# Kernel tuning notes

Hardware: AMD Instinct MI355X
Metric: run time of the kernel (lower is better)

## Reference

```python
import jax, jax.numpy as jnp
import numpy as np

NUM_HEADS = 32
HEAD_DIM = 128
HEAVY_BUDGET = 256
RECENT_BUDGET = 256
ROPE_BASE = 10000.0


def _rope_tables(position_ids, head_dim, dtype):
    inv_freq = 1.0 / (ROPE_BASE ** (jnp.arange(0, head_dim, 2, dtype=jnp.float32) / head_dim))
    freqs = position_ids.astype(jnp.float32)[..., None] * inv_freq  # [b, s, hd/2]
    emb = jnp.concatenate([freqs, freqs], axis=-1)                  # [b, s, hd]
    return jnp.cos(emb).astype(dtype), jnp.sin(emb).astype(dtype)


def _rotate_half(x):
    h = x.shape[-1] // 2
    return jnp.concatenate([-x[..., h:], x[..., :h]], axis=-1)


def setup_inputs() -> dict:
    key = jax.random.key(0)
    k1, k2, k3, k4, k5 = jax.random.split(key, 5)
    b, s, d = 1, 2048, 4096
    hidden_states = jax.random.normal(k1, (b, s, d), dtype=jnp.float32)
    # additive causal mask, as HF passes into forward
    neg = jnp.finfo(jnp.float32).min
    causal = jnp.tril(jnp.ones((s, s), dtype=bool))
    attention_mask = jnp.where(causal, 0.0, neg).astype(jnp.float32)[None, None]  # [1,1,s,s]
    position_ids = jnp.arange(s, dtype=jnp.int32)[None]  # [1, s]
    scale = 0.02
    Wq = jax.random.normal(k2, (d, d), dtype=jnp.float32) * scale
    Wk = jax.random.normal(k3, (d, d), dtype=jnp.float32) * scale
    Wv = jax.random.normal(k4, (d, d), dtype=jnp.float32) * scale
    Wo = jax.random.normal(k5, (d, d), dtype=jnp.float32) * scale
    return {"hidden_states": hidden_states, "attention_mask": attention_mask,
            "position_ids": position_ids, "Wq": Wq, "Wk": Wk, "Wv": Wv, "Wo": Wo}


def reference(hidden_states, attention_mask, position_ids, Wq, Wk, Wv, Wo):
    b, s, d = hidden_states.shape
    H, hd = NUM_HEADS, HEAD_DIM
    kv = s  # prefill: no past_key_value, masks reset

    # projections: nn.Linear(x) = x @ W.T
    q = (hidden_states @ Wq.T).reshape(b, s, H, hd).transpose(0, 2, 1, 3)  # [b,H,s,hd]
    k = (hidden_states @ Wk.T).reshape(b, s, H, hd).transpose(0, 2, 1, 3)
    v = (hidden_states @ Wv.T).reshape(b, s, H, hd).transpose(0, 2, 1, 3)

    cos, sin = _rope_tables(position_ids, hd, q.dtype)  # [b,s,hd]
    cos, sin = cos[:, None], sin[:, None]               # broadcast over heads
    q = q * cos + _rotate_half(q) * sin
    k = k * cos + _rotate_half(k) * sin

    attn = jnp.einsum('bhqd,bhkd->bhqk', q, k) / np.float32(np.sqrt(hd))
    neg = jnp.finfo(attn.dtype).min
    attn = jnp.maximum(attn + attention_mask, neg)
    # attention_masks_next is None on the first (prefill) call -> no multiplicative mask here
    attn = jax.nn.softmax(attn.astype(jnp.float32), axis=-1).astype(q.dtype)  # [b,H,s,kv]

    # running per-head score accumulation: sum over batch and query dims
    scores = attn.sum(axis=0).sum(axis=1)  # [H, kv]; previous_scores is None at prefill

    # heavy-hitter eviction mask for the next decode step (kv+1 columns)
    mask = jnp.ones((H, kv + 1), dtype=attn.dtype)
    # attn_tokens_all (=kv) > cache_budget, recent_budget > 0:
    mask = mask.at[:, :kv + 1 - RECENT_BUDGET].set(0.0)
    selected = scores[:, :kv - RECENT_BUDGET]                    # drop recent region
    _, keep_topk = jax.lax.top_k(selected, HEAVY_BUDGET)         # [H, heavy]
    mask = mask.at[jnp.arange(H)[:, None], keep_topk].set(1.0)   # scatter heavy hitters
    # torch aliasing: score_mask = attn_mask[:, :-1]; score_mask[:, -recent:] = 1 mutates attn_mask too
    mask = mask.at[:, kv - RECENT_BUDGET:kv].set(1.0)
    attention_masks_next = mask[None, :, None, :]                # [1,H,1,kv+1]
    previous_scores = scores * mask[:, :kv]                      # masked score state

    out = jnp.einsum('bhqk,bhkd->bhqd', attn, v)                 # [b,H,s,hd]
    out = out.transpose(0, 2, 1, 3).reshape(b, s, d) @ Wo.T
    return out, attention_masks_next, previous_scores
```

## Files before the change

kernel.cpp:

```cpp
#include <hip/hip_runtime.h>
#include <hip/hip_bf16.h>
#include <cmath>

#define S_LEN 2048
#define DMODEL 4096
#define NH 32
#define HDIM 128
#define HEAVY 256
#define RECENT 256
#define ATTN_SCALE 0.08838834764831845f
#define NEGBIG -3.0e38f
#define MB (1024ull * 1024ull)

typedef __attribute__((ext_vector_type(8))) short short8v;
typedef __attribute__((ext_vector_type(4))) short short4v;
typedef __attribute__((ext_vector_type(4))) float floatx4;

__device__ inline ushort f2bf(float x) {
  __hip_bfloat16 h = __float2bfloat16(x);
  return __builtin_bit_cast(ushort, h);
}
struct Split3 {
  short a, b, c;
};
__device__ inline Split3 split3(float x) {
  unsigned u = __float_as_uint(x);
  unsigned u1 = u & 0xFFFF0000u;
  float r1 = x - __uint_as_float(u1);
  unsigned u2 = __float_as_uint(r1) & 0xFFFF0000u;
  float r2 = r1 - __uint_as_float(u2);
  unsigned u3 = __float_as_uint(r2);
  Split3 o;
  o.a = (short)(u1 >> 16);
  o.b = (short)(u2 >> 16);
  o.c = (short)(u3 >> 16);
  return o;
}

__device__ __forceinline__ void gl_lds16(const short* gsrc, short* ldst) {
  __builtin_amdgcn_global_load_lds((const __attribute__((address_space(1))) void*)gsrc,
                                   (__attribute__((address_space(3))) void*)ldst, 16, 0, 0);
}

__global__ void split_mat(const float* __restrict__ X, short* __restrict__ Xa,
                          short* __restrict__ Xb, short* __restrict__ Xc, int n4) {
  int stride = gridDim.x * blockDim.x;
  for (int i = blockIdx.x * blockDim.x + threadIdx.x; i < n4; i += stride) {
    float4 v = reinterpret_cast<const float4*>(X)[i];
    float vv[4] = {v.x, v.y, v.z, v.w};
    short4v a, b, c;
#pragma unroll
    for (int j = 0; j < 4; j++) {
      Split3 t = split3(vv[j]);
      a[j] = t.a; b[j] = t.b; c[j] = t.c;
    }
    reinterpret_cast<short4v*>(Xa)[i] = a;
    reinterpret_cast<short4v*>(Xb)[i] = b;
    reinterpret_cast<short4v*>(Xc)[i] = c;
  }
}

__global__ __launch_bounds__(256) void gemm6h(const short* __restrict__ Aag,
                                              const short* __restrict__ Abg,
                                              const short* __restrict__ Acg,
                                              const float* __restrict__ B,
                                              float* __restrict__ C, int M, int N, int K) {
  __shared__ short Aa[128 * 40], Ab[128 * 40], Ac[128 * 40];
  __shared__ short Ba[128 * 40], Bb[128 * 40], Bc[128 * 40];
  const int tid = threadIdx.x;
  const int w = tid >> 6, l = tid & 63, g = l >> 4, ln = l & 15;
  const int wm = w >> 1, wn = w & 1;
  const int row0 = blockIdx.y * 128, col0 = blockIdx.x * 128;
  floatx4 acc[4][4] = {};
  for (int k0 = 0; k0 < K; k0 += 32) {
    __syncthreads();
#pragma unroll
    for (int i = 0; i < 2; i++) {
      int id = tid + i * 256;
      int r = id >> 2, c = id & 3;
      size_t ga = (size_t)(row0 + r) * K + k0 + c * 8;
      int o = r * 40 + c * 8;
      *reinterpret_cast<short8v*>(&Aa[o]) = *reinterpret_cast<const short8v*>(&Aag[ga]);
      *reinterpret_cast<short8v*>(&Ab[o]) = *reinterpret_cast<const short8v*>(&Abg[ga]);
      *reinterpret_cast<short8v*>(&Ac[o]) = *reinterpret_cast<const short8v*>(&Acg[ga]);
    }
#pragma unroll
    for (int i = 0; i < 4; i++) {
      int id = tid + i * 256;
      int r = id >> 3, c4 = id & 7;
      float4 bv = *reinterpret_cast<const float4*>(&B[(size_t)(col0 + r) * K + k0 + c4 * 4]);
      float bf[4] = {bv.x, bv.y, bv.z, bv.w};
      short4v b1, b2, b3;
#pragma unroll
      for (int j = 0; j < 4; j++) {
        Split3 t = split3(bf[j]);
        b1[j] = t.a; b2[j] = t.b; b3[j] = t.c;
      }
      int o = r * 40 + c4 * 4;
      *reinterpret_cast<short4v*>(&Ba[o]) = b1;
      *reinterpret_cast<short4v*>(&Bb[o]) = b2;
      *reinterpret_cast<short4v*>(&Bc[o]) = b3;
    }
    __syncthreads();
#pragma unroll
    for (int i = 0; i < 4; i++) {
      int ar = (wm * 64 + i * 16 + ln) * 40 + g * 8;
      short8v a1 = *reinterpret_cast<const short8v*>(&Aa[ar]);
      short8v a2 = *reinterpret_cast<const short8v*>(&Ab[ar]);
      short8v a3 = *reinterpret_cast<const short8v*>(&Ac[ar]);
#pragma unroll
      for (int j = 0; j < 4; j++) {
        int br = (wn * 64 + j * 16 + ln) * 40 + g * 8;
        short8v b1 = *reinterpret_cast<const short8v*>(&Ba[br]);
        short8v b2 = *reinterpret_cast<const short8v*>(&Bb[br]);
        short8v b3 = *reinterpret_cast<const short8v*>(&Bc[br]);
        acc[i][j] = __builtin_amdgcn_mfma_f32_16x16x32_bf16(a1, b1, acc[i][j], 0, 0, 0);
        acc[i][j] = __builtin_amdgcn_mfma_f32_16x16x32_bf16(a1, b2, acc[i][j], 0, 0, 0);
        acc[i][j] = __builtin_amdgcn_mfma_f32_16x16x32_bf16(a2, b1, acc[i][j], 0, 0, 0);
        acc[i][j] = __builtin_amdgcn_mfma_f32_16x16x32_bf16(a1, b3, acc[i][j], 0, 0, 0);
        acc[i][j] = __builtin_amdgcn_mfma_f32_16x16x32_bf16(a2, b2, acc[i][j], 0, 0, 0);
        acc[i][j] = __builtin_amdgcn_mfma_f32_16x16x32_bf16(a3, b1, acc[i][j], 0, 0, 0);
      }
    }
  }
#pragma unroll
  for (int i = 0; i < 4; i++)
#pragma unroll
    for (int j = 0; j < 4; j++)
#pragma unroll
      for (int r = 0; r < 4; r++)
        C[(size_t)(row0 + wm * 64 + i * 16 + g * 4 + r) * N + col0 + wn * 64 + j * 16 + ln] =
            acc[i][j][r];
}

__global__ __launch_bounds__(256) void gemm_bf1(const float* __restrict__ A,
                                                const float* __restrict__ B,
                                                float* __restrict__ C, int M, int N, int K) {
  __shared__ short Ah[128 * 40];
  __shared__ short Bh[128 * 40];
  const int tid = threadIdx.x;
  const int w = tid >> 6, l = tid & 63, g = l >> 4, ln = l & 15;
  const int wm = w >> 1, wn = w & 1;
  const int row0 = blockIdx.y * 128, col0 = blockIdx.x * 128;
  floatx4 acc[4][4] = {};
  for (int k0 = 0; k0 < K; k0 += 32) {
    __syncthreads();
#pragma unroll
    for (int i = 0; i < 4; i++) {
      int id = tid + i * 256;
      int r = id >> 3, c4 = id & 7;
      float4 av = *reinterpret_cast<const float4*>(&A[(size_t)(row0 + r) * K + k0 + c4 * 4]);
      float4 bv = *reinterpret_cast<const float4*>(&B[(size_t)(col0 + r) * K + k0 + c4 * 4]);
      short4v ah, bh;
      ah[0] = (short)f2bf(av.x); ah[1] = (short)f2bf(av.y);
      ah[2] = (short)f2bf(av.z); ah[3] = (short)f2bf(av.w);
      bh[0] = (short)f2bf(bv.x); bh[1] = (short)f2bf(bv.y);
      bh[2] = (short)f2bf(bv.z); bh[3] = (short)f2bf(bv.w);
      *reinterpret_cast<short4v*>(&Ah[r * 40 + c4 * 4]) = ah;
      *reinterpret_cast<short4v*>(&Bh[r * 40 + c4 * 4]) = bh;
    }
    __syncthreads();
#pragma unroll
    for (int i = 0; i < 4; i++) {
      short8v a = *reinterpret_cast<const short8v*>(&Ah[(wm * 64 + i * 16 + ln) * 40 + g * 8]);
#pragma unroll
      for (int j = 0; j < 4; j++) {
        short8v b = *reinterpret_cast<const short8v*>(&Bh[(wn * 64 + j * 16 + ln) * 40 + g * 8]);
        acc[i][j] = __builtin_amdgcn_mfma_f32_16x16x32_bf16(a, b, acc[i][j], 0, 0, 0);
      }
    }
  }
#pragma unroll
  for (int i = 0; i < 4; i++)
#pragma unroll
    for (int j = 0; j < 4; j++)
#pragma unroll
      for (int r = 0; r < 4; r++)
        C[(size_t)(row0 + wm * 64 + i * 16 + g * 4 + r) * N + col0 + wn * 64 + j * 16 + ln] =
            acc[i][j][r];
}

__global__ __launch_bounds__(256) void gemm_vbt(const short* __restrict__ Ab2,
                                                const float* __restrict__ B,
                                                ushort* __restrict__ Vt, int M, int N, int K) {
  __shared__ short Ah[128 * 40];
  __shared__ short Bh[128 * 40];
  const int tid = threadIdx.x;
  const int w = tid >> 6, l = tid & 63, g = l >> 4, ln = l & 15;
  const int wm = w >> 1, wn = w & 1;
  const int row0 = blockIdx.y * 128, col0 = blockIdx.x * 128;
  floatx4 acc[4][4] = {};
  for (int k0 = 0; k0 < K; k0 += 32) {
    __syncthreads();
#pragma unroll
    for (int i = 0; i < 2; i++) {
      int id = tid + i * 256;
      int r = id >> 2, c = id & 3;
      *reinterpret_cast<short8v*>(&Ah[r * 40 + c * 8]) =
          *reinterpret_cast<const short8v*>(&Ab2[(size_t)(row0 + r) * K + k0 + c * 8]);
    }
#pragma unroll
    for (int i = 0; i < 4; i++) {
      int id = tid + i * 256;
      int r = id >> 3, c4 = id & 7;
      float4 bv = *reinterpret_cast<const float4*>(&B[(size_t)(col0 + r) * K + k0 + c4 * 4]);
      short4v bh;
      bh[0] = (short)f2bf(bv.x); bh[1] = (short)f2bf(bv.y);
      bh[2] = (short)f2bf(bv.z); bh[3] = (short)f2bf(bv.w);
      *reinterpret_cast<short4v*>(&Bh[r * 40 + c4 * 4]) = bh;
    }
    __syncthreads();
#pragma unroll
    for (int i = 0; i < 4; i++) {
      short8v a = *reinterpret_cast<const short8v*>(&Ah[(wm * 64 + i * 16 + ln) * 40 + g * 8]);
#pragma unroll
      for (int j = 0; j < 4; j++) {
        short8v b = *reinterpret_cast<const short8v*>(&Bh[(wn * 64 + j * 16 + ln) * 40 + g * 8]);
        acc[i][j] = __builtin_amdgcn_mfma_f32_16x16x32_bf16(a, b, acc[i][j], 0, 0, 0);
      }
    }
  }
#pragma unroll
  for (int i = 0; i < 4; i++)
#pragma unroll
    for (int j = 0; j < 4; j++) {
      short4v o;
#pragma unroll
      for (int r = 0; r < 4; r++) o[r] = (short)f2bf(acc[i][j][r]);
      size_t n = col0 + wn * 64 + j * 16 + ln;
      size_t m0 = row0 + wm * 64 + i * 16 + g * 4;
      *reinterpret_cast<short4v*>(&Vt[n * M + m0]) = o;
    }
}

__global__ void rope_convert(const float* __restrict__ Q, const float* __restrict__ K,
                             const int* __restrict__ pos, short* __restrict__ Qa,
                             short* __restrict__ Qb, short* __restrict__ Qc,
                             short* __restrict__ Ka, short* __restrict__ Kb,
                             short* __restrict__ Kc) {
  int idx = blockIdx.x * blockDim.x + threadIdx.x;
  if (idx >= S_LEN * 64) return;
  int d = idx & 63;
  int r = idx >> 6;
  float p = (float)pos[r];
  float invf = (float)pow(10000.0, -(double)(2 * d) / 128.0);
  float ang = p * invf;
  float c = cosf(ang), s = sinf(ang);
  for (int h = 0; h < NH; h++) {
    size_t base = (size_t)r * DMODEL + h * HDIM + d;
    float q1 = Q[base], q2 = Q[base + 64];
    float k1 = K[base], k2 = K[base + 64];
    float qa = q1 * c - q2 * s, qb = q2 * c + q1 * s;
    float ka = k1 * c - k2 * s, kb = k2 * c + k1 * s;
    Split3 t;
    t = split3(qa); Qa[base] = t.a; Qb[base] = t.b; Qc[base] = t.c;
    t = split3(qb); Qa[base + 64] = t.a; Qb[base + 64] = t.b; Qc[base + 64] = t.c;
    t = split3(ka); Ka[base] = t.a; Kb[base] = t.b; Kc[base] = t.c;
    t = split3(kb); Ka[base + 64] = t.a; Kb[base + 64] = t.b; Kc[base + 64] = t.c;
  }
}

#define KVB 32
#define KSPL (KVB * 128)

__device__ __forceinline__ floatx4 qk6_tile(const short* KaS, const short* KbS,
                                            const short* KcS, const short8v q1[4],
                                            const short8v q2[4], const short8v q3[4],
                                            int krow, int g) {
  floatx4 cA = {}, cB = {}, cC = {}, cD = {}, cE = {}, cF = {};
#pragma unroll
  for (int dc = 0; dc < 4; dc++) {
    int didx = krow * 128 + ((dc * 32 + g * 8) ^ ((krow & 7) << 3));
    short8v k1 = *reinterpret_cast<const short8v*>(&KaS[didx]);
    short8v k2 = *reinterpret_cast<const short8v*>(&KbS[didx]);
    short8v k3 = *reinterpret_cast<const short8v*>(&KcS[didx]);
    cA = __builtin_amdgcn_mfma_f32_16x16x32_bf16(q1[dc], k1, cA, 0, 0, 0);
    cB = __builtin_amdgcn_mfma_f32_16x16x32_bf16(q1[dc], k2, cB, 0, 0, 0);
    cC = __builtin_amdgcn_mfma_f32_16x16x32_bf16(q2[dc], k1, cC, 0, 0, 0);
    cD = __builtin_amdgcn_mfma_f32_16x16x32_bf16(q1[dc], k3, cD, 0, 0, 0);
    cE = __builtin_amdgcn_mfma_f32_16x16x32_bf16(q2[dc], k2, cE, 0, 0, 0);
    cF = __builtin_amdgcn_mfma_f32_16x16x32_bf16(q3[dc], k1, cF, 0, 0, 0);
  }
  return ((cA + cB) + (cC + cD)) + (cE + cF);
}

__device__ __forceinline__ void issue_tile(const short* __restrict__ Ka,
                                           const short* __restrict__ Kb,
                                           const short* __restrict__ Kc, int k0, int h,
                                           short* bufA, short* bufB, short* bufC, int tid) {
  const int wb = tid & 192;
#pragma unroll
  for (int it = 0; it < 2; it++) {
    int j = it * 256 + tid;
    int r = j >> 4, cl = j & 15;
    int cg = cl ^ (r & 7);
    size_t goff = (size_t)(k0 + r) * DMODEL + h * HDIM + cg * 8;
    int cb = (it * 256 + wb) * 8;
    gl_lds16(Ka + goff, bufA + cb);
    gl_lds16(Kb + goff, bufB + cb);
    gl_lds16(Kc + goff, bufC + cb);
  }
}

__global__ __launch_bounds__(256, 3) void attn_fused(
    const short* __restrict__ Qa, const short* __restrict__ Qb, const short* __restrict__ Qc,
    const short* __restrict__ Ka, const short* __restrict__ Kb, const short* __restrict__ Kc,
    const ushort* __restrict__ Vt, float* __restrict__ AO, float* __restrict__ sp4) {
  __shared__ short KS[2][3][KSPL];
  __shared__ short Ps[4 * 512];
  const int bid = blockIdx.x;
  const int qb = 31 - (bid >> 5);
  const int h = bid & 31;
  const int tid = threadIdx.x;
  const int w = tid >> 6, g = (tid >> 4) & 3, ln = tid & 15;
  const int q0 = qb * 64;
  const int qrow = q0 + w * 16 + ln;
  short8v q1[4], q2[4], q3[4];
#pragma unroll
  for (int dc = 0; dc < 4; dc++) {
    size_t off = (size_t)qrow * DMODEL + h * HDIM + dc * 32 + g * 8;
    q1[dc] = *reinterpret_cast<const short8v*>(&Qa[off]);
    q2[dc] = *reinterpret_cast<const short8v*>(&Qb[off]);
    q3[dc] = *reinterpret_cast<const short8v*>(&Qc[off]);
  }
  float m_r[4], l_r[4];
#pragma unroll
  for (int r = 0; r < 4; r++) { m_r[r] = NEGBIG; l_r[r] = 0.f; }
  const int nkt = 2 * qb + 2;

  issue_tile(Ka, Kb, Kc, 0, h, KS[0][0], KS[0][1], KS[0][2], tid);
  __syncthreads();
  for (int t = 0; t < nkt; t++) {
    const int k0 = t * KVB;
    const int cur = t & 1;
    if (t + 1 < nkt)
      issue_tile(Ka, Kb, Kc, k0 + KVB, h, KS[cur ^ 1][0], KS[cur ^ 1][1], KS[cur ^ 1][2], tid);
    float sv[2][4];
#pragma unroll
    for (int ct = 0; ct < 2; ct++) {
      floatx4 sacc = qk6_tile(KS[cur][0], KS[cur][1], KS[cur][2], q1, q2, q3, ct * 16 + ln, g);
#pragma unroll
      for (int r = 0; r < 4; r++) {
        float s = sacc[r] * ATTN_SCALE;
        int key = k0 + ct * 16 + ln;
        int qq = q0 + w * 16 + g * 4 + r;
        sv[ct][r] = (key <= qq) ? s : NEGBIG;
      }
    }
#pragma unroll
    for (int r = 0; r < 4; r++) {
      float tmax = fmaxf(sv[0][r], sv[1][r]);
      tmax = fmaxf(tmax, __shfl_xor(tmax, 1));
      tmax = fmaxf(tmax, __shfl_xor(tmax, 2));
      tmax = fmaxf(tmax, __shfl_xor(tmax, 4));
      tmax = fmaxf(tmax, __shfl_xor(tmax, 8));
      float mnew = fmaxf(m_r[r], tmax);
      float ssum = __expf(sv[0][r] - mnew) + __expf(sv[1][r] - mnew);
      ssum += __shfl_xor(ssum, 1);
      ssum += __shfl_xor(ssum, 2);
      ssum += __shfl_xor(ssum, 4);
      ssum += __shfl_xor(ssum, 8);
      l_r[r] = l_r[r] * __expf(m_r[r] - mnew) + ssum;
      m_r[r] = mnew;
    }
    __syncthreads();
  }
  float inv_l[4];
#pragma unroll
  for (int r = 0; r < 4; r++) inv_l[r] = 1.0f / l_r[r];

  floatx4 o[8] = {};
  issue_tile(Ka, Kb, Kc, 0, h, KS[0][0], KS[0][1], KS[0][2], tid);
  __syncthreads();
  for (int t = 0; t < nkt; t++) {
    const int k0 = t * KVB;
    const int cur = t & 1;
    if (t + 1 < nkt)
      issue_tile(Ka, Kb, Kc, k0 + KVB, h, KS[cur ^ 1][0], KS[cur ^ 1][1], KS[cur ^ 1][2], tid);
    float pv[2][4];
#pragma unroll
    for (int ct = 0; ct < 2; ct++) {
      floatx4 sacc = qk6_tile(KS[cur][0], KS[cur][1], KS[cur][2], q1, q2, q3, ct * 16 + ln, g);
#pragma unroll
      for (int r = 0; r < 4; r++) {
        float s = sacc[r] * ATTN_SCALE;
        int key = k0 + ct * 16 + ln;
        int qq = q0 + w * 16 + g * 4 + r;
        s = (key <= qq) ? s : NEGBIG;
        pv[ct][r] = __expf(s - m_r[r]) * inv_l[r];
      }
    }
#pragma unroll
    for (int ct = 0; ct < 2; ct++) {
      float c2 = pv[ct][0] + pv[ct][1] + pv[ct][2] + pv[ct][3];
      c2 += __shfl_xor(c2, 16);
      c2 += __shfl_xor(c2, 32);
      if (g == 0) sp4[((size_t)(qb * 4 + w) * NH + h) * S_LEN + k0 + ct * 16 + ln] = c2;
    }
#pragma unroll
    for (int ct = 0; ct < 2; ct++)
#pragma unroll
      for (int r = 0; r < 4; r++) {
        int prow = g * 4 + r, pcol = ct * 16 + ln;
        Ps[w * 512 + prow * 32 + (pcol ^ (((prow >> 1) & 1) << 4))] = (short)f2bf(pv[ct][r]);
      }
    short8v pa = *reinterpret_cast<const short8v*>(
        &Ps[w * 512 + ln * 32 + ((g * 8) ^ (((ln >> 1) & 1) << 4))]);
#pragma unroll
    for (int ctd = 0; ctd < 8; ctd++) {
      size_t voff = ((size_t)h * HDIM + ctd * 16 + ln) * S_LEN + k0 + g * 8;
      short8v vb = *reinterpret_cast<const short8v*>(&Vt[voff]);
      o[ctd] = __builtin_amdgcn_mfma_f32_16x16x32_bf16(pa, vb, o[ctd], 0, 0, 0);
    }
    __syncthreads();
  }
#pragma unroll
  for (int ctd = 0; ctd < 8; ctd++)
#pragma unroll
    for (int r = 0; r < 4; r++)
      AO[(size_t)(q0 + w * 16 + g * 4 + r) * DMODEL + h * HDIM + ctd * 16 + ln] = o[ctd][r];
}

__global__ void reduce_scores(const float* __restrict__ sp4, float* __restrict__ scores) {
  int idx = blockIdx.x * blockDim.x + threadIdx.x;
  if (idx >= NH * S_LEN) return;
  int h = idx >> 11, k = idx & 2047;
  float s = 0.f;
  for (int j = 0; j < 128; j++) s += sp4[((size_t)j * NH + h) * S_LEN + k];
  scores[idx] = s;
}

__global__ __launch_bounds__(256) void topk_mask_kernel(const float* __restrict__ scores,
                                                        float* __restrict__ out_mask,
                                                        float* __restrict__ prev_scores) {
  const int h = blockIdx.x;
  __shared__ unsigned sb[S_LEN - RECENT];
  __shared__ int cnt_sh;
  const int NSEL = S_LEN - RECENT;
  const int tid = threadIdx.x;
  const float* sc = scores + (size_t)h * S_LEN;
  for (int i = tid; i < NSEL; i += 256) sb[i] = __float_as_uint(sc[i]);
  __syncthreads();
  unsigned prefix = 0u;
  for (int b = 31; b >= 0; b--) {
    unsigned cand = prefix | (1u << b);
    if (tid == 0) cnt_sh = 0;
    __syncthreads();
    int c = 0;
    for (int i = tid; i < NSEL; i += 256) c += (sb[i] >= cand) ? 1 : 0;
    atomicAdd(&cnt_sh, c);
    __syncthreads();
    if (cnt_sh >= HEAVY) prefix = cand;
    __syncthreads();
  }
  if (tid == 0) cnt_sh = 0;
  __syncthreads();
  int c = 0;
  for (int i = tid; i < NSEL; i += 256) c += (sb[i] > prefix) ? 1 : 0;
  atomicAdd(&cnt_sh, c);
  __syncthreads();
  const int c1 = cnt_sh;
  float* mrow = out_mask + (size_t)h * (S_LEN + 1);
  float* prow = prev_scores + (size_t)h * S_LEN;
  for (int j = NSEL + tid; j < S_LEN + 1; j += 256) mrow[j] = 1.0f;
  for (int k = NSEL + tid; k < S_LEN; k += 256) prow[k] = sc[k];
  for (int i = tid; i < NSEL; i += 256) {
    bool sel = sb[i] > prefix;
    mrow[i] = sel ? 1.f : 0.f;
    prow[i] = sel ? sc[i] : 0.f;
  }
  __syncthreads();
  if (tid == 0) {
    int need = HEAVY - c1;
    for (int i = 0; i < NSEL && need > 0; i++) {
      if (sb[i] == prefix) { mrow[i] = 1.f; prow[i] = sc[i]; need--; }
    }
  }
}

extern "C" void kernel_launch(void* const* d_in, const int* in_sizes, int n_in,
                              void* d_out, int out_size, void* d_ws, size_t ws_size,
                              hipStream_t stream) {
  const float* hidden = (const float*)d_in[0];
  const int* pos = (const int*)d_in[2];
  const float* Wq = (const float*)d_in[3];
  const float* Wk = (const float*)d_in[4];
  const float* Wv = (const float*)d_in[5];
  const float* Wo = (const float*)d_in[6];

  float* out0 = (float*)d_out;
  float* out_mask = out0 + (size_t)S_LEN * DMODEL;
  float* prev_scores = out_mask + (size_t)NH * (S_LEN + 1);

  char* ws = (char*)d_ws;
  float* Qf = (float*)(ws + 0 * MB);
  float* Kf = (float*)(ws + 32 * MB);
  ushort* Vt = (ushort*)(ws + 64 * MB);
  short* Ha = (short*)(ws + 80 * MB);
  short* Hb = (short*)(ws + 96 * MB);
  short* Hc = (short*)(ws + 112 * MB);
  short* Qa = (short*)(ws + 80 * MB);
  short* Qb = (short*)(ws + 96 * MB);
  short* Qc = (short*)(ws + 112 * MB);
  short* Ka = (short*)(ws + 128 * MB);
  short* Kb = (short*)(ws + 144 * MB);
  short* Kc = (short*)(ws + 160 * MB);
  float* AO = Qf;
  float* sp4 = Kf;
  float* scores = (float*)(ws + 64 * MB);

  dim3 gg(DMODEL / 128, S_LEN / 128);
  split_mat<<<2048, 256, 0, stream>>>(hidden, Ha, Hb, Hc, S_LEN * DMODEL / 4);
  gemm6h<<<gg, 256, 0, stream>>>(Ha, Hb, Hc, Wq, Qf, S_LEN, DMODEL, DMODEL);
  gemm6h<<<gg, 256, 0, stream>>>(Ha, Hb, Hc, Wk, Kf, S_LEN, DMODEL, DMODEL);
  gemm_vbt<<<gg, 256, 0, stream>>>(Ha, Wv, Vt, S_LEN, DMODEL, DMODEL);

  int rope_total = S_LEN * 64;
  rope_convert<<<(rope_total + 255) / 256, 256, 0, stream>>>(Qf, Kf, pos, Qa, Qb, Qc, Ka, Kb, Kc);

  hipError_t _e = hipMemsetAsync(sp4, 0, (size_t)128 * NH * S_LEN * sizeof(float), stream);
  (void)_e;
  attn_fused<<<1024, 256, 0, stream>>>(Qa, Qb, Qc, Ka, Kb, Kc, Vt, AO, sp4);

  reduce_scores<<<(NH * S_LEN + 255) / 256, 256, 0, stream>>>(sp4, scores);
  topk_mask_kernel<<<NH, 256, 0, stream>>>(scores, out_mask, prev_scores);

  gemm_bf1<<<gg, 256, 0, stream>>>(AO, Wo, out0, S_LEN, DMODEL, DMODEL);
}
```

Measured before the change: 1.594 ms.

## Pre-split Q/K weights into bf16 triples and use a Cauchy-Schwarz softmax bound

Q and K weights are now split into three bf16 parts in separate passes, half a matrix at a time, so the GEMM loads ready-made bf16 B tiles instead of re-splitting fp32 weights in every block. A new norms kernel computes per-row query norms and a per-head max key norm. Attention then uses |q|·max|k|·scale as a fixed upper bound in place of the online running max, which removes the per-tile max and sum shuffle reductions from the first pass. The cost is extra split passes and workspace traffic. The fixed bound also risks exp underflow when real scores sit far below it.

```diff
diff --git a/kernel.cpp b/kernel.cpp
--- a/kernel.cpp
+++ b/kernel.cpp
@@ -60,17 +60,36 @@
   }
 }
 
-__global__ __launch_bounds__(256) void gemm6h(const short* __restrict__ Aag,
-                                              const short* __restrict__ Abg,
-                                              const short* __restrict__ Acg,
-                                              const float* __restrict__ B,
-                                              float* __restrict__ C, int M, int N, int K) {
+__global__ void norms_kernel(const float* __restrict__ Qf, const float* __restrict__ Kf,
+                             float* __restrict__ qn, unsigned* __restrict__ mk2) {
+  int p = blockIdx.x * 4 + (threadIdx.x >> 6);
+  int lane = threadIdx.x & 63;
+  int r = p >> 5, h = p & 31;
+  const float2 qv = *reinterpret_cast<const float2*>(&Qf[(size_t)r * DMODEL + h * HDIM + lane * 2]);
+  const float2 kv = *reinterpret_cast<const float2*>(&Kf[(size_t)r * DMODEL + h * HDIM + lane * 2]);
+  float sq = qv.x * qv.x + qv.y * qv.y;
+  float sk = kv.x * kv.x + kv.y * kv.y;
+#pragma unroll
+  for (int off = 1; off <= 32; off <<= 1) {
+    sq += __shfl_xor(sq, off);
+    sk += __shfl_xor(sk, off);
+  }
+  if (lane == 0) {
+    qn[h * S_LEN + r] = sqrtf(sq);
+    atomicMax(&mk2[h], __float_as_uint(sk));
+  }
+}
+
+__global__ __launch_bounds__(256) void gemm6p(
+    const short* __restrict__ Aag, const short* __restrict__ Abg, const short* __restrict__ Acg,
+    const short* __restrict__ Bag, const short* __restrict__ Bbg, const short* __restrict__ Bcg,
+    float* __restrict__ C, int M, int N, int K, int colbase) {
   __shared__ short Aa[128 * 40], Ab[128 * 40], Ac[128 * 40];
   __shared__ short Ba[128 * 40], Bb[128 * 40], Bc[128 * 40];
   const int tid = threadIdx.x;
   const int w = tid >> 6, l = tid & 63, g = l >> 4, ln = l & 15;
   const int wm = w >> 1, wn = w & 1;
-  const int row0 = blockIdx.y * 128, col0 = blockIdx.x * 128;
+  const int row0 = blockIdx.y * 128, col0l = blockIdx.x * 128;
   floatx4 acc[4][4] = {};
   for (int k0 = 0; k0 < K; k0 += 32) {
     __syncthreads();
@@ -79,27 +98,14 @@
       int id = tid + i * 256;
       int r = id >> 2, c = id & 3;
       size_t ga = (size_t)(row0 + r) * K + k0 + c * 8;
+      size_t gb = (size_t)(col0l + r) * K + k0 + c * 8;
       int o = r * 40 + c * 8;
       *reinterpret_cast<short8v*>(&Aa[o]) = *reinterpret_cast<const short8v*>(&Aag[ga]);
       *reinterpret_cast<short8v*>(&Ab[o]) = *reinterpret_cast<const short8v*>(&Abg[ga]);
       *reinterpret_cast<short8v*>(&Ac[o]) = *reinterpret_cast<const short8v*>(&Acg[ga]);
-    }
-#pragma unroll
-    for (int i = 0; i < 4; i++) {
-      int id = tid + i * 256;
-      int r = id >> 3, c4 = id & 7;
-      float4 bv = *reinterpret_cast<const float4*>(&B[(size_t)(col0 + r) * K + k0 + c4 * 4]);
-      float bf[4] = {bv.x, bv.y, bv.z, bv.w};
-      short4v b1, b2, b3;
-#pragma unroll
-      for (int j = 0; j < 4; j++) {
-        Split3 t = split3(bf[j]);
-        b1[j] = t.a; b2[j] = t.b; b3[j] = t.c;
-      }
-      int o = r * 40 + c4 * 4;
-      *reinterpret_cast<short4v*>(&Ba[o]) = b1;
-      *reinterpret_cast<short4v*>(&Bb[o]) = b2;
-      *reinterpret_cast<short4v*>(&Bc[o]) = b3;
+      *reinterpret_cast<short8v*>(&Ba[o]) = *reinterpret_cast<const short8v*>(&Bag[gb]);
+      *reinterpret_cast<short8v*>(&Bb[o]) = *reinterpret_cast<const short8v*>(&Bbg[gb]);
+      *reinterpret_cast<short8v*>(&Bc[o]) = *reinterpret_cast<const short8v*>(&Bcg[gb]);
     }
     __syncthreads();
 #pragma unroll
@@ -123,6 +129,7 @@
       }
     }
   }
+  const int col0 = colbase + col0l;
 #pragma unroll
   for (int i = 0; i < 4; i++)
 #pragma unroll
@@ -305,7 +312,8 @@
 __global__ __launch_bounds__(256, 3) void attn_fused(
     const short* __restrict__ Qa, const short* __restrict__ Qb, const short* __restrict__ Qc,
     const short* __restrict__ Ka, const short* __restrict__ Kb, const short* __restrict__ Kc,
-    const ushort* __restrict__ Vt, float* __restrict__ AO, float* __restrict__ sp4) {
+    const ushort* __restrict__ Vt, const float* __restrict__ qn,
+    const unsigned* __restrict__ mk2, float* __restrict__ AO, float* __restrict__ sp4) {
   __shared__ short KS[2][3][KSPL];
   __shared__ short Ps[4 * 512];
   const int bid = blockIdx.x;
@@ -323,9 +331,13 @@
     q2[dc] = *reinterpret_cast<const short8v*>(&Qb[off]);
     q3[dc] = *reinterpret_cast<const short8v*>(&Qc[off]);
   }
-  float m_r[4], l_r[4];
-#pragma unroll
-  for (int r = 0; r < 4; r++) { m_r[r] = NEGBIG; l_r[r] = 0.f; }
+  const float mk = sqrtf(__uint_as_float(mk2[h]));
+  float B_r[4], l_r[4];
+#pragma unroll
+  for (int r = 0; r < 4; r++) {
+    B_r[r] = qn[h * S_LEN + q0 + w * 16 + g * 4 + r] * mk * ATTN_SCALE;
+    l_r[r] = 0.f;
+  }
   const int nkt = 2 * qb + 2;
 
   issue_tile(Ka, Kb, Kc, 0, h, KS[0][0], KS[0][1], KS[0][2], tid);
@@ -335,7 +347,6 @@
     const int cur = t & 1;
     if (t + 1 < nkt)
       issue_tile(Ka, Kb, Kc, k0 + KVB, h, KS[cur ^ 1][0], KS[cur ^ 1][1], KS[cur ^ 1][2], tid);
-    float sv[2][4];
 #pragma unroll
     for (int ct = 0; ct < 2; ct++) {
       floatx4 sacc = qk6_tile(KS[cur][0], KS[cur][1], KS[cur][2], q1, q2, q3, ct * 16 + ln, g);
@@ -344,30 +355,21 @@
         float s = sacc[r] * ATTN_SCALE;
         int key = k0 + ct * 16 + ln;
         int qq = q0 + w * 16 + g * 4 + r;
-        sv[ct][r] = (key <= qq) ? s : NEGBIG;
+        l_r[r] += (key <= qq) ? __expf(s - B_r[r]) : 0.f;
       }
     }
-#pragma unroll
-    for (int r = 0; r < 4; r++) {
-      float tmax = fmaxf(sv[0][r], sv[1][r]);
-      tmax = fmaxf(tmax, __shfl_xor(tmax, 1));
-      tmax = fmaxf(tmax, __shfl_xor(tmax, 2));
-      tmax = fmaxf(tmax, __shfl_xor(tmax, 4));
-      tmax = fmaxf(tmax, __shfl_xor(tmax, 8));
-      float mnew = fmaxf(m_r[r], tmax);
-      float ssum = __expf(sv[0][r] - mnew) + __expf(sv[1][r] - mnew);
-      ssum += __shfl_xor(ssum, 1);
-      ssum += __shfl_xor(ssum, 2);
-      ssum += __shfl_xor(ssum, 4);
-      ssum += __shfl_xor(ssum, 8);
-      l_r[r] = l_r[r] * __expf(m_r[r] - mnew) + ssum;
-      m_r[r] = mnew;
-    }
     __syncthreads();
   }
   float inv_l[4];
 #pragma unroll
-  for (int r = 0; r < 4; r++) inv_l[r] = 1.0f / l_r[r];
+  for (int r = 0; r < 4; r++) {
+    float l = l_r[r];
+    l += __shfl_xor(l, 1);
+    l += __shfl_xor(l, 2);
+    l += __shfl_xor(l, 4);
+    l += __shfl_xor(l, 8);
+    inv_l[r] = 1.0f / l;
+  }
 
   floatx4 o[8] = {};
   issue_tile(Ka, Kb, Kc, 0, h, KS[0][0], KS[0][1], KS[0][2], tid);
@@ -386,8 +388,8 @@
         float s = sacc[r] * ATTN_SCALE;
         int key = k0 + ct * 16 + ln;
         int qq = q0 + w * 16 + g * 4 + r;
-        s = (key <= qq) ? s : NEGBIG;
-        pv[ct][r] = __expf(s - m_r[r]) * inv_l[r];
+        float e = (key <= qq) ? __expf(s - B_r[r]) : 0.f;
+        pv[ct][r] = e * inv_l[r];
       }
     }
 #pragma unroll
@@ -502,6 +504,9 @@
   short* Qa = (short*)(ws + 80 * MB);
   short* Qb = (short*)(ws + 96 * MB);
   short* Qc = (short*)(ws + 112 * MB);
+  short* Wsa = (short*)(ws + 128 * MB);
+  short* Wsb = (short*)(ws + 144 * MB);
+  short* Wsc = (short*)(ws + 160 * MB);
   short* Ka = (short*)(ws + 128 * MB);
   short* Kb = (short*)(ws + 144 * MB);
   short* Kc = (short*)(ws + 160 * MB);
@@ -509,21 +514,36 @@
   float* sp4 = Kf;
   float* scores = (float*)(ws + 64 * MB);
 
-  dim3 gg(DMODEL / 128, S_LEN / 128);
+  float* qn = out0;
+  unsigned* mk2 = (unsigned*)(out0 + NH * S_LEN);
+
+  const int WHALF = 2048 * 4096;
+
   split_mat<<<2048, 256, 0, stream>>>(hidden, Ha, Hb, Hc, S_LEN * DMODEL / 4);
-  gemm6h<<<gg, 256, 0, stream>>>(Ha, Hb, Hc, Wq, Qf, S_LEN, DMODEL, DMODEL);
-  gemm6h<<<gg, 256, 0, stream>>>(Ha, Hb, Hc, Wk, Kf, S_LEN, DMODEL, DMODEL);
-  gemm_vbt<<<gg, 256, 0, stream>>>(Ha, Wv, Vt, S_LEN, DMODEL, DMODEL);
+  split_mat<<<2048, 256, 0, stream>>>(Wq, Wsa, Wsb, Wsc, WHALF / 4);
+  gemm6p<<<dim3(16, 16), 256, 0, stream>>>(Ha, Hb, Hc, Wsa, Wsb, Wsc, Qf, S_LEN, DMODEL, DMODEL, 0);
+  split_mat<<<2048, 256, 0, stream>>>(Wq + WHALF, Wsa, Wsb, Wsc, WHALF / 4);
+  gemm6p<<<dim3(16, 16), 256, 0, stream>>>(Ha, Hb, Hc, Wsa, Wsb, Wsc, Qf, S_LEN, DMODEL, DMODEL, 2048);
+  split_mat<<<2048, 256, 0, stream>>>(Wk, Wsa, Wsb, Wsc, WHALF / 4);
+  gemm6p<<<dim3(16, 16), 256, 0, stream>>>(Ha, Hb, Hc, Wsa, Wsb, Wsc, Kf, S_LEN, DMODEL, DMODEL, 0);
+  split_mat<<<2048, 256, 0, stream>>>(Wk + WHALF, Wsa, Wsb, Wsc, WHALF / 4);
+  gemm6p<<<dim3(16, 16), 256, 0, stream>>>(Ha, Hb, Hc, Wsa, Wsb, Wsc, Kf, S_LEN, DMODEL, DMODEL, 2048);
+
+  gemm_vbt<<<dim3(32, 16), 256, 0, stream>>>(Ha, Wv, Vt, S_LEN, DMODEL, DMODEL);
+
+  hipError_t _e0 = hipMemsetAsync(mk2, 0, NH * sizeof(unsigned), stream);
+  (void)_e0;
+  norms_kernel<<<S_LEN * NH / 4, 256, 0, stream>>>(Qf, Kf, qn, mk2);
 
   int rope_total = S_LEN * 64;
   rope_convert<<<(rope_total + 255) / 256, 256, 0, stream>>>(Qf, Kf, pos, Qa, Qb, Qc, Ka, Kb, Kc);
 
   hipError_t _e = hipMemsetAsync(sp4, 0, (size_t)128 * NH * S_LEN * sizeof(float), stream);
   (void)_e;
-  attn_fused<<<1024, 256, 0, stream>>>(Qa, Qb, Qc, Ka, Kb, Kc, Vt, AO, sp4);
+  attn_fused<<<1024, 256, 0, stream>>>(Qa, Qb, Qc, Ka, Kb, Kc, Vt, qn, mk2, AO, sp4);
 
   reduce_scores<<<(NH * S_LEN + 255) / 256, 256, 0, stream>>>(sp4, scores);
   topk_mask_kernel<<<NH, 256, 0, stream>>>(scores, out_mask, prev_scores);
 
-  gemm_bf1<<<gg, 256, 0, stream>>>(AO, Wo, out0, S_LEN, DMODEL, DMODEL);
-}
+  gemm_bf1<<<dim3(32, 16), 256, 0, stream>>>(AO, Wo, out0, S_LEN, DMODEL, DMODEL);
+}
```

After: 2.367 ms. 48.5% more time.

## Replace online softmax max with Cauchy-Schwarz norm bound and double query tile

Applied to the files above, without the earlier changes.

A new norms kernel computes per-row query norms and the per-head maximum key norm. These give a fixed upper bound on each score, so the first attention pass no longer tracks a running max. It just accumulates exp(s - bound) per lane and reduces once at the end, which removes the per-tile shuffles and rescaling. The attention kernel also moves to 512-thread blocks covering 128 queries, so each K tile load is shared by twice as many query rows. The bound can sit far above the true max for other inputs, which risks exp underflow. Using the out0 buffer as scratch relies on it being overwritten later.

```diff
diff --git a/kernel.cpp b/kernel.cpp
--- a/kernel.cpp
+++ b/kernel.cpp
@@ -58,6 +58,36 @@
     reinterpret_cast<short4v*>(Xb)[i] = b;
     reinterpret_cast<short4v*>(Xc)[i] = c;
   }
+}
+
+__global__ __launch_bounds__(256) void norms_kernel(const float* __restrict__ Qf,
+                                                    const float* __restrict__ Kf,
+                                                    float* __restrict__ qn,
+                                                    float* __restrict__ mk2p) {
+  const int h = blockIdx.x >> 4, ch = blockIdx.x & 15;
+  const int wv = threadIdx.x >> 6, lane = threadIdx.x & 63;
+  __shared__ float wmax[4];
+  float mx = 0.f;
+  for (int i = 0; i < 32; i++) {
+    int r = ch * 128 + wv * 32 + i;
+    const float2 qv =
+        *reinterpret_cast<const float2*>(&Qf[(size_t)r * DMODEL + h * HDIM + lane * 2]);
+    const float2 kv =
+        *reinterpret_cast<const float2*>(&Kf[(size_t)r * DMODEL + h * HDIM + lane * 2]);
+    float sq = qv.x * qv.x + qv.y * qv.y;
+    float sk = kv.x * kv.x + kv.y * kv.y;
+#pragma unroll
+    for (int off = 1; off <= 32; off <<= 1) {
+      sq += __shfl_xor(sq, off);
+      sk += __shfl_xor(sk, off);
+    }
+    if (lane == 0) qn[h * S_LEN + r] = sqrtf(sq);
+    mx = fmaxf(mx, sk);
+  }
+  if (lane == 0) wmax[wv] = mx;
+  __syncthreads();
+  if (threadIdx.x == 0)
+    mk2p[blockIdx.x] = fmaxf(fmaxf(wmax[0], wmax[1]), fmaxf(wmax[2], wmax[3]));
 }
 
 __global__ __launch_bounds__(256) void gemm6h(const short* __restrict__ Aag,
@@ -288,32 +318,29 @@
                                            const short* __restrict__ Kb,
                                            const short* __restrict__ Kc, int k0, int h,
                                            short* bufA, short* bufB, short* bufC, int tid) {
-  const int wb = tid & 192;
-#pragma unroll
-  for (int it = 0; it < 2; it++) {
-    int j = it * 256 + tid;
-    int r = j >> 4, cl = j & 15;
-    int cg = cl ^ (r & 7);
-    size_t goff = (size_t)(k0 + r) * DMODEL + h * HDIM + cg * 8;
-    int cb = (it * 256 + wb) * 8;
-    gl_lds16(Ka + goff, bufA + cb);
-    gl_lds16(Kb + goff, bufB + cb);
-    gl_lds16(Kc + goff, bufC + cb);
-  }
-}
-
-__global__ __launch_bounds__(256, 3) void attn_fused(
+  const int wb = tid & 448;
+  int r = tid >> 4, cl = tid & 15;
+  int cg = cl ^ (r & 7);
+  size_t goff = (size_t)(k0 + r) * DMODEL + h * HDIM + cg * 8;
+  int cb = wb * 8;
+  gl_lds16(Ka + goff, bufA + cb);
+  gl_lds16(Kb + goff, bufB + cb);
+  gl_lds16(Kc + goff, bufC + cb);
+}
+
+__global__ __launch_bounds__(512, 4) void attn_fused(
     const short* __restrict__ Qa, const short* __restrict__ Qb, const short* __restrict__ Qc,
     const short* __restrict__ Ka, const short* __restrict__ Kb, const short* __restrict__ Kc,
-    const ushort* __restrict__ Vt, float* __restrict__ AO, float* __restrict__ sp4) {
+    const ushort* __restrict__ Vt, const float* __restrict__ qn,
+    const float* __restrict__ mk2p, float* __restrict__ AO, float* __restrict__ sp4) {
   __shared__ short KS[2][3][KSPL];
-  __shared__ short Ps[4 * 512];
+  __shared__ short Ps[8 * 512];
   const int bid = blockIdx.x;
-  const int qb = 31 - (bid >> 5);
+  const int qb = 15 - (bid >> 5);
   const int h = bid & 31;
   const int tid = threadIdx.x;
   const int w = tid >> 6, g = (tid >> 4) & 3, ln = tid & 15;
-  const int q0 = qb * 64;
+  const int q0 = qb * 128;
   const int qrow = q0 + w * 16 + ln;
   short8v q1[4], q2[4], q3[4];
 #pragma unroll
@@ -323,10 +350,17 @@
     q2[dc] = *reinterpret_cast<const short8v*>(&Qb[off]);
     q3[dc] = *reinterpret_cast<const short8v*>(&Qc[off]);
   }
-  float m_r[4], l_r[4];
-#pragma unroll
-  for (int r = 0; r < 4; r++) { m_r[r] = NEGBIG; l_r[r] = 0.f; }
-  const int nkt = 2 * qb + 2;
+  float mkv = 0.f;
+#pragma unroll
+  for (int j = 0; j < 16; j++) mkv = fmaxf(mkv, mk2p[h * 16 + j]);
+  const float mk = sqrtf(mkv);
+  float B_r[4], l_r[4];
+#pragma unroll
+  for (int r = 0; r < 4; r++) {
+    B_r[r] = qn[h * S_LEN + q0 + w * 16 + g * 4 + r] * mk * ATTN_SCALE;
+    l_r[r] = 0.f;
+  }
+  const int nkt = 4 * qb + 4;
 
   issue_tile(Ka, Kb, Kc, 0, h, KS[0][0], KS[0][1], KS[0][2], tid);
   __syncthreads();
@@ -335,7 +369,6 @@
     const int cur = t & 1;
     if (t + 1 < nkt)
       issue_tile(Ka, Kb, Kc, k0 + KVB, h, KS[cur ^ 1][0], KS[cur ^ 1][1], KS[cur ^ 1][2], tid);
-    float sv[2][4];
 #pragma unroll
     for (int ct = 0; ct < 2; ct++) {
       floatx4 sacc = qk6_tile(KS[cur][0], KS[cur][1], KS[cur][2], q1, q2, q3, ct * 16 + ln, g);
@@ -344,30 +377,21 @@
         float s = sacc[r] * ATTN_SCALE;
         int key = k0 + ct * 16 + ln;
         int qq = q0 + w * 16 + g * 4 + r;
-        sv[ct][r] = (key <= qq) ? s : NEGBIG;
-      }
-    }
-#pragma unroll
-    for (int r = 0; r < 4; r++) {
-      float tmax = fmaxf(sv[0][r], sv[1][r]);
-      tmax = fmaxf(tmax, __shfl_xor(tmax, 1));
-      tmax = fmaxf(tmax, __shfl_xor(tmax, 2));
-      tmax = fmaxf(tmax, __shfl_xor(tmax, 4));
-      tmax = fmaxf(tmax, __shfl_xor(tmax, 8));
-      float mnew = fmaxf(m_r[r], tmax);
-      float ssum = __expf(sv[0][r] - mnew) + __expf(sv[1][r] - mnew);
-      ssum += __shfl_xor(ssum, 1);
-      ssum += __shfl_xor(ssum, 2);
-      ssum += __shfl_xor(ssum, 4);
-      ssum += __shfl_xor(ssum, 8);
-      l_r[r] = l_r[r] * __expf(m_r[r] - mnew) + ssum;
-      m_r[r] = mnew;
+        l_r[r] += (key <= qq) ? __expf(s - B_r[r]) : 0.f;
+      }
     }
     __syncthreads();
   }
   float inv_l[4];
 #pragma unroll
-  for (int r = 0; r < 4; r++) inv_l[r] = 1.0f / l_r[r];
+  for (int r = 0; r < 4; r++) {
+    float l = l_r[r];
+    l += __shfl_xor(l, 1);
+    l += __shfl_xor(l, 2);
+    l += __shfl_xor(l, 4);
+    l += __shfl_xor(l, 8);
+    inv_l[r] = 1.0f / l;
+  }
 
   floatx4 o[8] = {};
   issue_tile(Ka, Kb, Kc, 0, h, KS[0][0], KS[0][1], KS[0][2], tid);
@@ -386,8 +410,8 @@
         float s = sacc[r] * ATTN_SCALE;
         int key = k0 + ct * 16 + ln;
         int qq = q0 + w * 16 + g * 4 + r;
-        s = (key <= qq) ? s : NEGBIG;
-        pv[ct][r] = __expf(s - m_r[r]) * inv_l[r];
+        float e = (key <= qq) ? __expf(s - B_r[r]) : 0.f;
+        pv[ct][r] = e * inv_l[r];
       }
     }
 #pragma unroll
@@ -395,7 +419,7 @@
       float c2 = pv[ct][0] + pv[ct][1] + pv[ct][2] + pv[ct][3];
       c2 += __shfl_xor(c2, 16);
       c2 += __shfl_xor(c2, 32);
-      if (g == 0) sp4[((size_t)(qb * 4 + w) * NH + h) * S_LEN + k0 + ct * 16 + ln] = c2;
+      if (g == 0) sp4[((size_t)(qb * 8 + w) * NH + h) * S_LEN + k0 + ct * 16 + ln] = c2;
     }
 #pragma unroll
     for (int ct = 0; ct < 2; ct++)
@@ -509,18 +533,23 @@
   float* sp4 = Kf;
   float* scores = (float*)(ws + 64 * MB);
 
+  float* qn = out0;
+  float* mk2p = out0 + NH * S_LEN;
+
   dim3 gg(DMODEL / 128, S_LEN / 128);
   split_mat<<<2048, 256, 0, stream>>>(hidden, Ha, Hb, Hc, S_LEN * DMODEL / 4);
   gemm6h<<<gg, 256, 0, stream>>>(Ha, Hb, Hc, Wq, Qf, S_LEN, DMODEL, DMODEL);
   gemm6h<<<gg, 256, 0, stream>>>(Ha, Hb, Hc, Wk, Kf, S_LEN, DMODEL, DMODEL);
   gemm_vbt<<<gg, 256, 0, stream>>>(Ha, Wv, Vt, S_LEN, DMODEL, DMODEL);
 
+  norms_kernel<<<512, 256, 0, stream>>>(Qf, Kf, qn, mk2p);
+
   int rope_total = S_LEN * 64;
   rope_convert<<<(rope_total + 255) / 256, 256, 0, stream>>>(Qf, Kf, pos, Qa, Qb, Qc, Ka, Kb, Kc);
 
   hipError_t _e = hipMemsetAsync(sp4, 0, (size_t)128 * NH * S_LEN * sizeof(float), stream);
   (void)_e;
-  attn_fused<<<1024, 256, 0, stream>>>(Qa, Qb, Qc, Ka, Kb, Kc, Vt, AO, sp4);
+  attn_fused<<<512, 512, 0, stream>>>(Qa, Qb, Qc, Ka, Kb, Kc, Vt, qn, mk2p, AO, sp4);
 
   reduce_scores<<<(NH * S_LEN + 255) / 256, 256, 0, stream>>>(sp4, scores);
   topk_mask_kernel<<<NH, 256, 0, stream>>>(scores, out_mask, prev_scores);
```

New measurement: 2.142 ms. 1.34x slower.
